# Performance work log

Measured on AMD Instinct MI355X. Metric: run time of the kernel, lower is better.

Reference implementation:

```python
import jax, jax.numpy as jnp
import numpy as np

# Module constants (from init_kwargs / defaults)
OUT_SIZE = (4, 32, 32)      # (Z, X, Y) grid
REAL_SIZE = (3.0, 25.0, 25.0)
SCALE = 1.4
THRESHOLD = 0.5
D_ELEMS = np.array([0.74 * SCALE, 0.528 * SCALE], dtype=np.float32)  # per-element match/NMS radius (O, H)


def _transform(x):
    """(B, X, Y, Z, 4*E) -> coords (B, E, N, 3), conf (B, E, N); N = Z*X*Y."""
    B, X, Y, Z, L = x.shape
    E = L // 4
    v = x.reshape(B, X, Y, Z, E, 4).transpose(0, 4, 3, 1, 2, 5)   # (B,E,Z,X,Y,4)
    v = v[..., jnp.array([2, 0, 1, 3])]                            # reorder last dim
    Zs, Xs, Ys = OUT_SIZE
    ind = jnp.stack(jnp.meshgrid(jnp.arange(Zs), jnp.arange(Xs), jnp.arange(Ys), indexing='ij'),
                    axis=-1).astype(x.dtype)                       # (Z,X,Y,3) == torch nonzero of ones
    expand = jnp.array([r / o for o, r in zip(OUT_SIZE, REAL_SIZE)], dtype=x.dtype)
    coords = (v[..., :3] + ind) * expand
    conf = v[..., 3]
    N = Zs * Xs * Ys
    return coords.reshape(B, E, N, 3), conf.reshape(B, E, N)


def _sort_by_conf(coords, conf):
    order = jnp.argsort(-conf, axis=-1)
    coords = jnp.take_along_axis(coords, order[..., None], axis=2)
    conf = jnp.take_along_axis(conf, order, axis=-1)
    return coords, conf


def _nms(pts, valid, d):
    """Greedy sequential NMS on one (N,3) point set. Point b is suppressed if any
    still-selected earlier point a<b lies within distance d. Invalid points never suppress."""
    N = pts.shape[0]
    d2 = jnp.sum((pts[:, None, :] - pts[None, :, :]) ** 2, axis=-1)   # (N,N)
    ar = jnp.arange(N)
    M = (d2 < d * d) & valid[:, None] & valid[None, :] & (ar[:, None] < ar[None, :])

    def body(b, sel):
        return sel.at[b].set(~jnp.any(sel & M[:, b]))

    sel = jax.lax.fori_loop(0, N, body, jnp.ones((N,), bool))
    return sel & valid


def _match(P, T, keepP, keepT, d):
    """Greedy row-major bipartite matching: each pred (in order) grabs the first
    still-unmatched target within distance d. Returns (TP, FP, FN) masks."""
    N = P.shape[0]
    d2 = jnp.sum((P[:, None, :] - T[None, :, :]) ** 2, axis=-1)      # (N,N)
    D = (d2 < d * d) & keepP[:, None] & keepT[None, :]

    def body(a, carry):
        selP, selT = carry
        avail = D[a] & ~selT
        has = jnp.any(avail)
        j = jnp.argmax(avail)                    # first available target index
        selT = selT.at[j].set(selT[j] | has)
        selP = selP.at[a].set(has)
        return (selP, selT)

    selP, selT = jax.lax.fori_loop(0, N, body,
                                   (jnp.zeros((N,), bool), jnp.zeros((N,), bool)))
    return selP, keepP & ~selP, keepT & ~selT    # TP, FP, FN masks


def setup_inputs() -> dict:
    key = jax.random.key(0)
    k1, k2 = jax.random.split(key)
    B = 4
    predictions = jax.random.normal(k1, (B, 32, 32, 4, 8), dtype=jnp.float32)
    targets = jax.random.normal(k2, (B, 32, 32, 4, 8), dtype=jnp.float32)
    return {"predictions": predictions, "targets": targets}


def reference(predictions, targets):
    Pc, Pconf = _sort_by_conf(*_transform(predictions))   # (B,E,N,3), (B,E,N)
    Tc, Tconf = _sort_by_conf(*_transform(targets))
    validP = Pconf > THRESHOLD
    validT = Tconf > THRESHOLD
    d = jnp.asarray(D_ELEMS)                               # (E,)

    nms_be = jax.vmap(jax.vmap(_nms, in_axes=(0, 0, 0)), in_axes=(0, 0, None))
    keepP = nms_be(Pc, validP, d)                          # (B,E,N) bool
    keepT = nms_be(Tc, validT, d)

    match_be = jax.vmap(jax.vmap(_match, in_axes=(0, 0, 0, 0, 0)), in_axes=(0, 0, 0, 0, None))
    tp, fp, fn = match_be(Pc, Tc, keepP, keepT, d)         # (B,E,N) bool each

    # sorted real-space points, NMS-kept masks, and TP/FP/FN masks (fixed-shape
    # equivalents of the torch module's filtered P/T/TP/FP/FN lists)
    return Pc, Tc, keepP, keepT, tp, fp, fn
```

## Files before the change

### kernel.cpp

```cpp
#include <hip/hip_runtime.h>
#include <hip/hip_bf16.h>

#pragma clang fp contract(off)

#define NPTS 4096
#define BE   8
#define COORD_SZ (BE * NPTS * 3)
#define MASK_SZ  (BE * NPTS)
#define OFF_PC   0
#define OFF_TC   (COORD_SZ)
#define OFF_KP   (2 * COORD_SZ)
#define OFF_KT   (2 * COORD_SZ + MASK_SZ)
#define OFF_TP   (2 * COORD_SZ + 2 * MASK_SZ)
#define OFF_FP   (2 * COORD_SZ + 3 * MASK_SZ)
#define OFF_FN   (2 * COORD_SZ + 4 * MASK_SZ)

#define VCAP 1664
#define NW   26

#define WS_V_OFF     524288ull
#define WS_KEEP_OFF  524352ull
#define WS_PP_OFF    528448ull
#define WS_PT_OFF    6066240ull
#define WS_NEED      8835136ull

#define NBC 16

typedef unsigned long long u64;

__device__ __forceinline__ float get_dd(int e) {
    const float d0 = (float)(0.74 * 1.4);
    const float d1 = (float)(0.528 * 1.4);
    float d = (e == 0) ? d0 : d1;
    return d * d;
}

__global__ __launch_bounds__(1024)
void sort_kernel(const float* __restrict__ pred,
                 const float* __restrict__ targ,
                 float* __restrict__ out,
                 int* __restrict__ Vcnt) {
    __shared__ u64 bufA[NPTS], bufB[NPTS];
    __shared__ unsigned int hist[1024];
    __shared__ unsigned int offarr[1024];
    __shared__ int wsum[16];
    __shared__ int vtot;
    const int s = blockIdx.x;
    const int arr = s & 1, be = s >> 1;
    const int b = be >> 1, e = be & 1;
    const float* __restrict__ src = arr ? targ : pred;
    const int t = threadIdx.x;
    const int lane = t & 63, wv = t >> 6;

    if (t == 0) vtot = 0;
    for (int n = t; n < NPTS; n += 1024) {
        int z = n >> 10, r = n & 1023, x = r >> 5, y = r & 31;
        int base = (((b * 32 + x) * 32 + y) * 4 + z) * 8 + e * 4;
        float conf = src[base + 3];
        unsigned int bits = __float_as_uint(conf);
        unsigned int u = (bits & 0x80000000u) ? ~bits : (bits | 0x80000000u);
        bufA[n] = ((u64)(~u) << 32) | (unsigned int)n;
    }
    __syncthreads();

    const u64 lmask = (1ull << lane) - 1ull;
    for (int k = 0; k < 8; ++k) {
        u64* cur = (k & 1) ? bufB : bufA;
        u64* nxt = (k & 1) ? bufA : bufB;
        const int shift = 32 + (k << 2);
        hist[t] = 0u;
        __syncthreads();

        u64 item[4]; int dg[4]; int rnk[4];
        #pragma unroll
        for (int m = 0; m < 4; ++m) {
            u64 it = cur[m * 1024 + t];
            int d = (int)((it >> shift) & 15);
            u64 eq = ~0ull;
            #pragma unroll
            for (int bb = 0; bb < 4; ++bb) {
                u64 bal = __ballot((d >> bb) & 1);
                eq &= ((d >> bb) & 1) ? bal : ~bal;
            }
            int r = (int)__popcll(eq & lmask);
            if (r == 0) hist[d * 64 + m * 16 + wv] = (unsigned int)__popcll(eq);
            item[m] = it; dg[m] = d; rnk[m] = r;
        }
        __syncthreads();

        {
            int v = (int)hist[t];
            int inc = v;
            #pragma unroll
            for (int dd = 1; dd < 64; dd <<= 1) {
                int x2 = __shfl_up(inc, dd);
                if (lane >= dd) inc += x2;
            }
            if (lane == 63) wsum[wv] = inc;
            __syncthreads();
            if (t < 16) {
                int wtot = wsum[t]; int iv = wtot;
                #pragma unroll
                for (int dd = 1; dd < 16; dd <<= 1) {
                    int x2 = __shfl_up(iv, dd);
                    if (t >= dd) iv += x2;
                }
                wsum[t] = iv - wtot;
            }
            __syncthreads();
            offarr[t] = (unsigned int)(wsum[wv] + (inc - v));
        }
        __syncthreads();

        #pragma unroll
        for (int m = 0; m < 4; ++m) {
            int pos = (int)offarr[dg[m] * 64 + m * 16 + wv] + rnk[m];
            nxt[pos] = item[m];
        }
        __syncthreads();
    }

    int myv = 0;
    for (int p = t; p < NPTS; p += 1024) {
        u64 key = bufA[p];
        int n = (int)(key & 0xFFFFFFFFull);
        myv += ((unsigned int)(key >> 32) < 0x40FFFFFFu) ? 1 : 0;
        int z = n >> 10, rr = n & 1023, x = rr >> 5, y = rr & 31;
        int base = (((b * 32 + x) * 32 + y) * 4 + z) * 8 + e * 4;
        float r0 = src[base + 0], r1 = src[base + 1], r2 = src[base + 2];
        float c0 = (r2 + (float)z) * 0.75f;
        float c1 = (r0 + (float)x) * 0.78125f;
        float c2 = (r1 + (float)y) * 0.78125f;
        float* dst = out + (size_t)arr * COORD_SZ + ((size_t)be * NPTS + p) * 3;
        dst[0] = c0; dst[1] = c1; dst[2] = c2;
    }
    atomicAdd(&vtot, myv);
    __syncthreads();
    if (t == 0) Vcnt[s] = vtot;
}

__global__ __launch_bounds__(256)
void matrix_kernel(const float* __restrict__ out,
                   const int* __restrict__ Vcnt,
                   u64* __restrict__ ws64) {
    __shared__ float4 tcol[VCAP];
    __shared__ float rowc[64][3];
    const int bx = blockIdx.x;
    const int j = bx / 26, c = bx % 26;
    const int t = threadIdx.x;

    int sRow, sCol, e;
    u64* dstBase;
    if (j < 16) {
        sRow = j; sCol = j; e = (j >> 1) & 1;
        dstBase = ws64 + (WS_PP_OFF / 8) + (size_t)j * VCAP * NW;
    } else {
        int be = j - 16;
        sRow = be * 2 + 0; sCol = be * 2 + 1; e = be & 1;
        dstBase = ws64 + (WS_PT_OFF / 8) + (size_t)be * VCAP * NW;
    }
    int Vr = Vcnt[sRow]; if (Vr > VCAP) Vr = VCAP;
    int Vc = Vcnt[sCol]; if (Vc > VCAP) Vc = VCAP;
    const int rb = c * 64;
    if (rb >= Vr) return;
    const float dd = get_dd(e);

    const float* __restrict__ colc = out + (size_t)(sCol & 1) * COORD_SZ + (size_t)(sCol >> 1) * NPTS * 3;
    const float* __restrict__ rowp = out + (size_t)(sRow & 1) * COORD_SZ + (size_t)(sRow >> 1) * NPTS * 3;

    for (int idx = t; idx < Vc * 3; idx += 256) {
        float v = colc[idx];
        int p = idx / 3, k = idx % 3;
        ((float*)&tcol[p])[k] = v;
    }
    for (int idx = t; idx < 192; idx += 256) {
        int i = idx / 3, k = idx % 3;
        if (rb + i < Vr) rowc[i][k] = rowp[(rb + i) * 3 + k];
    }
    __syncthreads();

    const int NWc = (Vc + 63) >> 6;
    const int wlimit = (j < 16) ? (c + 1) : NWc;
    const int i = t & 63;
    const bool rowOK = (rb + i) < Vr;
    if (rowOK) {
        float ax = rowc[i][0], ay = rowc[i][1], az = rowc[i][2];
        for (int w = t >> 6; w < wlimit; w += 4) {
            int jbase = w << 6;
            int jmax = Vc - jbase; if (jmax > 64) jmax = 64;
            u64 m = 0ull;
            for (int jj = 0; jj < jmax; ++jj) {
                float4 tc = tcol[jbase + jj];
                float dx = ax - tc.x, dy = ay - tc.y, dz = az - tc.z;
                float d2 = dx * dx + dy * dy + dz * dz;
                m |= (d2 < dd) ? (1ull << jj) : 0ull;
            }
            dstBase[(size_t)w * VCAP + (rb + i)] = m;
        }
    }
}

__global__ __launch_bounds__(1024)
void nms_rounds_kernel(float* __restrict__ out,
                       const int* __restrict__ Vcnt,
                       u64* __restrict__ ws64) {
    __shared__ unsigned short nbr[VCAP][NBC];
    __shared__ unsigned short nbrcnt[VCAP];
    __shared__ u64 U[NW];
    __shared__ u64 K[NW];
    __shared__ int remaining;
    const int s = blockIdx.x;
    const int arr = s & 1, be = s >> 1;
    const int t = threadIdx.x;
    int V = Vcnt[s]; if (V > VCAP) V = VCAP;
    const u64* __restrict__ Mx = ws64 + (WS_PP_OFF / 8) + (size_t)s * VCAP * NW;

    if (t < NW) {
        int rem = V - (t << 6);
        U[t] = (rem >= 64) ? ~0ull : ((rem > 0) ? ((1ull << rem) - 1ull) : 0ull);
        K[t] = 0ull;
    }
    if (t == 0) remaining = V;
    __syncthreads();

    bool dec0 = false, dec1 = false;
    #pragma unroll
    for (int half = 0; half < 2; ++half) {
        const int i = t + half * 1024;
        if (i < V) {
            const int wi = i >> 6;
            int cnt = 0;
            for (int w = 0; w <= wi; ++w) {
                u64 m = Mx[(size_t)w * VCAP + i];
                if (w == wi) m &= (1ull << (i & 63)) - 1ull;
                while (m) {
                    int bb = (int)__builtin_ctzll(m); m &= m - 1ull;
                    if (cnt < NBC) nbr[i][cnt] = (unsigned short)((w << 6) + bb);
                    cnt++;
                }
            }
            nbrcnt[i] = (unsigned short)cnt;
            if (cnt == 0) { if (half == 0) dec0 = true; else dec1 = true; }
        }
    }
    __syncthreads();
    {
        int ndec = 0;
        if (dec0) {
            const int i = t;
            atomicAnd(&U[i >> 6], ~(1ull << (i & 63)));
            atomicOr(&K[i >> 6], 1ull << (i & 63));
            ndec++;
        }
        if (dec1) {
            const int i = t + 1024;
            atomicAnd(&U[i >> 6], ~(1ull << (i & 63)));
            atomicOr(&K[i >> 6], 1ull << (i & 63));
            ndec++;
        }
        if (ndec) atomicSub(&remaining, ndec);
    }
    __syncthreads();

    while (remaining > 0) {
        bool d0 = false, k0 = false, d1 = false, k1 = false;
        #pragma unroll
        for (int half = 0; half < 2; ++half) {
            const int i = t + half * 1024;
            if (i < V && ((U[i >> 6] >> (i & 63)) & 1ull)) {
                bool cu = false, ck = false;
                int cnt = nbrcnt[i];
                if (cnt <= NBC) {
                    for (int k = 0; k < cnt; ++k) {
                        int j = nbr[i][k];
                        u64 bit = 1ull << (j & 63);
                        cu = cu || ((U[j >> 6] & bit) != 0ull);
                        ck = ck || ((K[j >> 6] & bit) != 0ull);
                    }
                } else {
                    const int wi = i >> 6;
                    u64 cuw = 0ull, ckw = 0ull;
                    for (int w = 0; w <= wi; ++w) {
                        u64 m = Mx[(size_t)w * VCAP + i];
                        if (w == wi) m &= (1ull << (i & 63)) - 1ull;
                        cuw |= m & U[w];
                        ckw |= m & K[w];
                    }
                    cu = cuw != 0ull; ck = ckw != 0ull;
                }
                if (!cu) {
                    if (half == 0) { d0 = true; k0 = !ck; }
                    else           { d1 = true; k1 = !ck; }
                }
            }
        }
        __syncthreads();

        int ndec = 0;
        if (d0) {
            const int i = t;
            atomicAnd(&U[i >> 6], ~(1ull << (i & 63)));
            if (k0) atomicOr(&K[i >> 6], 1ull << (i & 63));
            ndec++;
        }
        if (d1) {
            const int i = t + 1024;
            atomicAnd(&U[i >> 6], ~(1ull << (i & 63)));
            if (k1) atomicOr(&K[i >> 6], 1ull << (i & 63));
            ndec++;
        }
        if (ndec) atomicSub(&remaining, ndec);
        __syncthreads();
    }

    u64* kb = ws64 + (WS_KEEP_OFF / 8) + s * 32;
    if (t < 32) kb[t] = (t < NW) ? K[t] : 0ull;
    const size_t kbase = (arr == 0 ? OFF_KP : OFF_KT) + (size_t)be * NPTS;
    for (int p = t; p < NPTS; p += 1024) {
        bool k = (p < V) && ((K[p >> 6] >> (p & 63)) & 1ull);
        out[kbase + p] = k ? 1.0f : 0.0f;
    }
}

__global__ __launch_bounds__(1024)
void match_resolve_kernel(float* __restrict__ out,
                          const int* __restrict__ Vcnt,
                          u64* __restrict__ ws64) {
    __shared__ unsigned short cand[VCAP][16];
    __shared__ unsigned short candcnt[VCAP];
    __shared__ unsigned short rowlist[VCAP];
    __shared__ unsigned int colmin[VCAP];
    __shared__ u64 kPw[NW], kTw[NW], availT[NW];
    __shared__ int wp[NW];
    __shared__ int Mcnt, remaining;
    __shared__ unsigned int selP32[128];
    const int be = blockIdx.x;
    const int t = threadIdx.x;
    int Vp = Vcnt[be * 2 + 0]; if (Vp > VCAP) Vp = VCAP;
    int Vt = Vcnt[be * 2 + 1]; if (Vt > VCAP) Vt = VCAP;
    const int NWt = (Vt + 63) >> 6;
    const u64* __restrict__ PT = ws64 + (WS_PT_OFF / 8) + (size_t)be * VCAP * NW;

    if (t < NW) {
        kPw[t] = ws64[(WS_KEEP_OFF / 8) + (be * 2 + 0) * 32 + t];
        kTw[t] = ws64[(WS_KEEP_OFF / 8) + (be * 2 + 1) * 32 + t];
    }
    if (t < 128) selP32[t] = 0u;
    for (int idx = t; idx < VCAP; idx += 1024) colmin[idx] = 0xFFFFFFFFu;
    __syncthreads();

    if (t < 64) {
        int cP = (t < NW) ? __popcll(kPw[t]) : 0;
        int o = cP;
        for (int d = 1; d < 64; d <<= 1) {
            int v = __shfl_up(o, d);
            if (t >= d) o += v;
        }
        if (t < NW) wp[t] = o - cP;
        if (t == NW - 1) Mcnt = o;
    }
    __syncthreads();
    const int M = Mcnt;

    for (int a = t; a < Vp; a += 1024) {
        int w = a >> 6, bb = a & 63;
        u64 word = kPw[w];
        if ((word >> bb) & 1ull) {
            int pos = wp[w] + __popcll(word & ((1ull << bb) - 1ull));
            rowlist[pos] = (unsigned short)a;
        }
    }
    if (t < NW) availT[t] = kTw[t];
    if (t == 0) remaining = M;
    __syncthreads();

    #pragma unroll
    for (int half = 0; half < 2; ++half) {
        int g = t + half * 1024;
        if (g < M) {
            const int a = rowlist[g];
            int cnt = 0;
            for (int w = 0; w < NWt; ++w) {
                u64 m = PT[(size_t)w * VCAP + a] & kTw[w];
                while (m) {
                    int bb = (int)__builtin_ctzll(m); m &= m - 1ull;
                    if (cnt < 16) cand[g][cnt] = (unsigned short)((w << 6) + bb);
                    cnt++;
                }
            }
            candcnt[g] = (unsigned short)(cnt > 16 ? 16 : cnt);
        }
    }
    __syncthreads();

    bool und0 = (t < M);
    bool und1 = (t + 1024 < M);
    int round = 0;

    while (remaining > 0) {
        const unsigned int stampBase = (unsigned int)(4095 - round) << 11;
        int jt0 = -1, jt1 = -1;
        bool dead0 = false, dead1 = false;
        if (und0) {
            const int g = t;
            int cn = candcnt[g];
            for (int k = 0; k < cn; ++k) {
                int j = cand[g][k];
                if ((availT[j >> 6] >> (j & 63)) & 1ull) {
                    if (jt0 < 0) jt0 = j;
                    atomicMin(&colmin[j], stampBase | (unsigned int)g);
                }
            }
            if (jt0 < 0) dead0 = true;
        }
        if (und1) {
            const int g = t + 1024;
            int cn = candcnt[g];
            for (int k = 0; k < cn; ++k) {
                int j = cand[g][k];
                if ((availT[j >> 6] >> (j & 63)) & 1ull) {
                    if (jt1 < 0) jt1 = j;
                    atomicMin(&colmin[j], stampBase | (unsigned int)g);
                }
            }
            if (jt1 < 0) dead1 = true;
        }
        __syncthreads();

        int ndec = 0;
        if (und0) {
            const int g = t;
            if (dead0) { und0 = false; ndec++; }
            else if (colmin[jt0] == (stampBase | (unsigned int)g)) {
                atomicAnd(&availT[jt0 >> 6], ~(1ull << (jt0 & 63)));
                int a = rowlist[g];
                atomicOr(&selP32[a >> 5], 1u << (a & 31));
                und0 = false; ndec++;
            }
        }
        if (und1) {
            const int g = t + 1024;
            if (dead1) { und1 = false; ndec++; }
            else if (colmin[jt1] == (stampBase | (unsigned int)g)) {
                atomicAnd(&availT[jt1 >> 6], ~(1ull << (jt1 & 63)));
                int a = rowlist[g];
                atomicOr(&selP32[a >> 5], 1u << (a & 31));
                und1 = false; ndec++;
            }
        }
        if (ndec) atomicSub(&remaining, ndec);
        ++round;
        __syncthreads();
    }

    for (int n = t; n < NPTS; n += 1024) {
        int w = n >> 6;
        bool kpb = (w < NW) && ((kPw[w] >> (n & 63)) & 1ull);
        bool tpb = (selP32[n >> 5] >> (n & 31)) & 1u;
        bool fnb = (w < NW) && ((availT[w] >> (n & 63)) & 1ull);
        size_t o = (size_t)be * NPTS + n;
        out[OFF_TP + o] = tpb ? 1.0f : 0.0f;
        out[OFF_FP + o] = (kpb && !tpb) ? 1.0f : 0.0f;
        out[OFF_FN + o] = fnb ? 1.0f : 0.0f;
    }
}

#define FVCAP 2048
#define FNWMAX (FVCAP / 64)

__global__ __launch_bounds__(1024)
void sortnms_fallback(const float* __restrict__ pred,
                      const float* __restrict__ targ,
                      float* __restrict__ out,
                      u64* __restrict__ keepbits) {
    __shared__ u64 skey[NPTS];
    __shared__ float px[FVCAP], py[FVCAP], pz[FVCAP];
    __shared__ u64 kept[FNWMAX];
    __shared__ u64 mchunk[64];
    __shared__ int supp[64];
    __shared__ int vcnt;
    const int blk = blockIdx.x;
    const int arr = blk & 1;
    const int be  = blk >> 1;
    const int b = be >> 1, e = be & 1;
    const float* __restrict__ src = arr ? targ : pred;
    const int t = threadIdx.x;
    const float dd = get_dd(e);
    if (t == 0) vcnt = 0;

    for (int n = t; n < NPTS; n += 1024) {
        int z = n >> 10, r = n & 1023, x = r >> 5, y = r & 31;
        int base = (((b * 32 + x) * 32 + y) * 4 + z) * 8 + e * 4;
        float conf = src[base + 3];
        unsigned int bits = __float_as_uint(conf);
        unsigned int u = (bits & 0x80000000u) ? ~bits : (bits | 0x80000000u);
        skey[n] = ((u64)(~u) << 32) | (unsigned int)n;
    }
    __syncthreads();
    for (int k = 2; k <= NPTS; k <<= 1) {
        for (int j = k >> 1; j > 0; j >>= 1) {
            for (int i = t; i < NPTS; i += 1024) {
                int ixj = i ^ j;
                if (ixj > i) {
                    u64 a = skey[i], c = skey[ixj];
                    bool up = ((i & k) == 0);
                    if ((a > c) == up) { skey[i] = c; skey[ixj] = a; }
                }
            }
            __syncthreads();
        }
    }
    int myv = 0;
    for (int p = t; p < NPTS; p += 1024) {
        u64 key = skey[p];
        int n = (int)(key & 0xFFFFFFFFu);
        unsigned int u = ~(unsigned int)(key >> 32);
        myv += (u > 0xBF000000u) ? 1 : 0;
        int z = n >> 10, r = n & 1023, x = r >> 5, y = r & 31;
        int base = (((b * 32 + x) * 32 + y) * 4 + z) * 8 + e * 4;
        float r0 = src[base + 0], r1 = src[base + 1], r2 = src[base + 2];
        float c0 = (r2 + (float)z) * 0.75f;
        float c1 = (r0 + (float)x) * 0.78125f;
        float c2 = (r1 + (float)y) * 0.78125f;
        float* dst = out + (size_t)arr * COORD_SZ + ((size_t)be * NPTS + p) * 3;
        dst[0] = c0; dst[1] = c1; dst[2] = c2;
        if (p < FVCAP) { px[p] = c0; py[p] = c1; pz[p] = c2; }
    }
    atomicAdd(&vcnt, myv);
    if (t < FNWMAX) kept[t] = 0ull;
    __syncthreads();

    int V = vcnt; if (V > FVCAP) V = FVCAP;
    const int nchunks = (V + 63) >> 6;
    for (int c = 0; c < nchunks; ++c) {
        if (t < 64) supp[t] = 0;
        __syncthreads();
        {
            int i = t & 63, s = t >> 6;
            int p = (c << 6) + i;
            if (p < V) {
                float x = px[p], y = py[p], z = pz[p];
                int lim = c << 6;
                bool f = false;
                for (int j = s; j < lim; j += 16) {
                    if ((kept[j >> 6] >> (j & 63)) & 1ull) {
                        float dx = x - px[j], dy = y - py[j], dz = z - pz[j];
                        float d2 = dx * dx + dy * dy + dz * dz;
                        if (d2 < dd) { f = true; break; }
                    }
                }
                if (f) atomicOr(&supp[i], 1);
            }
        }
        __syncthreads();
        if (t < 64) {
            int p = (c << 6) + t;
            u64 m = 0ull;
            if (p < V) {
                float x = px[p], y = py[p], z = pz[p];
                for (int j = 0; j < t; ++j) {
                    int q = (c << 6) + j;
                    float dx = x - px[q], dy = y - py[q], dz = z - pz[q];
                    float d2 = dx * dx + dy * dy + dz * dz;
                    if (d2 < dd) m |= (1ull << j);
                }
            }
            mchunk[t] = m;
        }
        __syncthreads();
        if (t == 0) {
            u64 kw = 0ull;
            int lim = V - (c << 6); if (lim > 64) lim = 64;
            for (int i = 0; i < lim; ++i) {
                bool ki = (supp[i] == 0) && ((mchunk[i] & kw) == 0ull);
                if (ki) kw |= (1ull << i);
            }
            kept[c] = kw;
        }
        __syncthreads();
    }
    const size_t kbase = (arr == 0 ? OFF_KP : OFF_KT) + (size_t)be * NPTS;
    for (int p = t; p < NPTS; p += 1024) {
        bool kb = (p < V) && ((kept[(p >> 6) & (FNWMAX - 1)] >> (p & 63)) & 1ull);
        out[kbase + p] = kb ? 1.0f : 0.0f;
    }
    if (t < 64) keepbits[blk * 64 + t] = (t < FNWMAX) ? kept[t] : 0ull;
}

__global__ __launch_bounds__(1024)
void match_fallback(float* __restrict__ out,
                    const u64* __restrict__ keepbits) {
    __shared__ float tx[FVCAP], ty[FVCAP], tz[FVCAP];
    __shared__ unsigned short tj[FVCAP];
    __shared__ unsigned short aidx[FVCAP];
    __shared__ unsigned short matchPos[FVCAP];
    __shared__ u64 Mask[64][FNWMAX + 1];
    __shared__ u64 kPm[64], kTm[64];
    __shared__ unsigned int selP32[128], selT32[128];
    __shared__ int wpT[64], wpP[64];
    __shared__ int Mcnt2, Kcnt2;
    __shared__ float pcx[64], pcy[64], pcz[64];
    const int be = blockIdx.x;
    const int e = be & 1;
    const int t = threadIdx.x;
    const float dd = get_dd(e);
    const float* __restrict__ Pc = out + OFF_PC + (size_t)be * NPTS * 3;
    const float* __restrict__ Tc = out + OFF_TC + (size_t)be * NPTS * 3;

    if (t < 64) {
        kPm[t] = keepbits[(be * 2 + 0) * 64 + t];
        kTm[t] = keepbits[(be * 2 + 1) * 64 + t];
    }
    if (t < 128) { selP32[t] = 0u; selT32[t] = 0u; }
    __syncthreads();
    if (t < 64) {
        int cT = __popcll(kTm[t]), cP = __popcll(kPm[t]);
        int oT = cT, oP = cP;
        for (int d = 1; d < 64; d <<= 1) {
            int vT = __shfl_up(oT, d);
            int vP = __shfl_up(oP, d);
            if (t >= d) { oT += vT; oP += vP; }
        }
        wpT[t] = oT - cT;
        wpP[t] = oP - cP;
        if (t == 63) {
            Kcnt2 = (oT > FVCAP) ? FVCAP : oT;
            Mcnt2 = (oP > FVCAP) ? FVCAP : oP;
        }
    }
    __syncthreads();
    const int K = Kcnt2, M = Mcnt2;
    for (int n = t; n < NPTS; n += 1024) {
        int w = n >> 6, bb = n & 63;
        u64 bit = 1ull << bb, lowm = bit - 1ull;
        u64 wT = kTm[w], wP = kPm[w];
        if (wT & bit) {
            int pos = wpT[w] + __popcll(wT & lowm);
            if (pos < FVCAP) {
                tx[pos] = Tc[n * 3 + 0];
                ty[pos] = Tc[n * 3 + 1];
                tz[pos] = Tc[n * 3 + 2];
                tj[pos] = (unsigned short)n;
            }
        }
        if (wP & bit) {
            int pos = wpP[w] + __popcll(wP & lowm);
            if (pos < FVCAP) aidx[pos] = (unsigned short)n;
        }
    }
    __syncthreads();

    const int NWc = (K + 63) >> 6;
    const int nchunks = (M + 63) >> 6;
    u64 selTw = 0ull;

    for (int c = 0; c < nchunks; ++c) {
        int cnt = M - (c << 6); if (cnt > 64) cnt = 64;
        if (t < 64 && t < cnt) {
            int a = aidx[(c << 6) + t];
            pcx[t] = Pc[a * 3 + 0];
            pcy[t] = Pc[a * 3 + 1];
            pcz[t] = Pc[a * 3 + 2];
        }
        __syncthreads();
        {
            int i = t & 63, s = t >> 6;
            if (i < cnt) {
                float ax = pcx[i], ay = pcy[i], az = pcz[i];
                for (int w = s; w < NWc; w += 16) {
                    int jmax = K - (w << 6); if (jmax > 64) jmax = 64;
                    int base = w << 6;
                    u64 m = 0ull;
                    for (int jj = 0; jj < jmax; ++jj) {
                        float dx = ax - tx[base + jj];
                        float dy = ay - ty[base + jj];
                        float dz = az - tz[base + jj];
                        float d2 = dx * dx + dy * dy + dz * dz;
                        m |= (d2 < dd) ? (1ull << jj) : 0ull;
                    }
                    Mask[i][w] = m;
                }
            }
        }
        __syncthreads();
        if (t < 64) {
            u64 mnext = (cnt > 0 && t < NWc) ? Mask[0][t] : 0ull;
            for (int i = 0; i < cnt; ++i) {
                u64 mrow = mnext;
                mnext = (i + 1 < cnt && t < NWc) ? Mask[i + 1][t] : 0ull;
                u64 avail = mrow & ~selTw;
                u64 bal = __ballot(avail != 0ull);
                if (bal) {
                    int w0 = (int)__builtin_ctzll(bal);
                    if (t == w0) {
                        int bb = (int)__builtin_ctzll(avail);
                        selTw |= 1ull << bb;
                        matchPos[(c << 6) + i] = (unsigned short)((w0 << 6) + bb);
                    }
                } else if (t == 0) {
                    matchPos[(c << 6) + i] = 0xffffu;
                }
            }
        }
        __syncthreads();
    }
    for (int g = t; g < M; g += 1024) {
        unsigned short pos = matchPos[g];
        if (pos != 0xffffu) {
            int jj = tj[pos];
            int a  = aidx[g];
            atomicOr(&selT32[jj >> 5], 1u << (jj & 31));
            atomicOr(&selP32[a >> 5],  1u << (a & 31));
        }
    }
    __syncthreads();
    for (int n = t; n < NPTS; n += 1024) {
        bool kpb = (kPm[n >> 6] >> (n & 63)) & 1ull;
        bool ktb = (kTm[n >> 6] >> (n & 63)) & 1ull;
        bool tpb = (selP32[n >> 5] >> (n & 31)) & 1u;
        bool stb = (selT32[n >> 5] >> (n & 31)) & 1u;
        size_t o = (size_t)be * NPTS + n;
        out[OFF_TP + o] = tpb ? 1.0f : 0.0f;
        out[OFF_FP + o] = (kpb && !tpb) ? 1.0f : 0.0f;
        out[OFF_FN + o] = (ktb && !stb) ? 1.0f : 0.0f;
    }
}

extern "C" void kernel_launch(void* const* d_in, const int* in_sizes, int n_in,
                              void* d_out, int out_size, void* d_ws, size_t ws_size,
                              hipStream_t stream) {
    const float* pred = (const float*)d_in[0];
    const float* targ = (const float*)d_in[1];
    float* out = (float*)d_out;

    if (ws_size >= WS_NEED) {
        int* Vcnt = (int*)((char*)d_ws + WS_V_OFF);
        u64* ws64 = (u64*)d_ws;

        sort_kernel<<<16, 1024, 0, stream>>>(pred, targ, out, Vcnt);
        matrix_kernel<<<624, 256, 0, stream>>>(out, Vcnt, ws64);
        nms_rounds_kernel<<<16, 1024, 0, stream>>>(out, Vcnt, ws64);
        match_resolve_kernel<<<8, 1024, 0, stream>>>(out, Vcnt, ws64);
    } else {
        u64* keepbits = (u64*)d_ws;
        sortnms_fallback<<<16, 1024, 0, stream>>>(pred, targ, out, keepbits);
        match_fallback<<<8, 1024, 0, stream>>>(out, keepbits);
    }
}
```

Baseline: 161.2 us.

## Use per-point byte state with in-round updates in NMS rounds kernel

Replaces the shared U/K bitmasks in the NMS rounds loop with a volatile per-point byte state (undecided, kept, suppressed). Points write their decision as soon as they make it, so later points in the same round can see it. A point is now suppressed as soon as any earlier neighbour is kept, without waiting for every neighbour to be decided. This drops one barrier per round, removes the 64-bit atomics, and should need fewer rounds. The keep bitmask is rebuilt with wave ballots at the end. The risk is that correctness now depends on state changes only ever moving forward and on volatile visibility across waves.

```diff
diff --git a/kernel.cpp b/kernel.cpp
--- a/kernel.cpp
+++ b/kernel.cpp
@@ -206,24 +206,21 @@
                        u64* __restrict__ ws64) {
     __shared__ unsigned short nbr[VCAP][NBC];
     __shared__ unsigned short nbrcnt[VCAP];
-    __shared__ u64 U[NW];
-    __shared__ u64 K[NW];
+    __shared__ unsigned char stbuf[VCAP];
     __shared__ int remaining;
+    volatile unsigned char* st = stbuf;
     const int s = blockIdx.x;
     const int arr = s & 1, be = s >> 1;
     const int t = threadIdx.x;
     int V = Vcnt[s]; if (V > VCAP) V = VCAP;
     const u64* __restrict__ Mx = ws64 + (WS_PP_OFF / 8) + (size_t)s * VCAP * NW;
 
-    if (t < NW) {
-        int rem = V - (t << 6);
-        U[t] = (rem >= 64) ? ~0ull : ((rem > 0) ? ((1ull << rem) - 1ull) : 0ull);
-        K[t] = 0ull;
-    }
+    for (int i = t; i < VCAP; i += 1024) stbuf[i] = 0;
     if (t == 0) remaining = V;
     __syncthreads();
 
-    bool dec0 = false, dec1 = false;
+    bool und0 = (t < V), und1 = (t + 1024 < V);
+    int ndec1 = 0;
     #pragma unroll
     for (int half = 0; half < 2; ++half) {
         const int i = t + half * 1024;
@@ -240,84 +237,67 @@
                 }
             }
             nbrcnt[i] = (unsigned short)cnt;
-            if (cnt == 0) { if (half == 0) dec0 = true; else dec1 = true; }
-        }
-    }
-    __syncthreads();
-    {
+            if (cnt == 0) {
+                st[i] = 1;
+                if (half == 0) und0 = false; else und1 = false;
+                ndec1++;
+            }
+        }
+    }
+    if (ndec1) atomicSub(&remaining, ndec1);
+    __syncthreads();
+
+    while (remaining > 0) {
         int ndec = 0;
-        if (dec0) {
-            const int i = t;
-            atomicAnd(&U[i >> 6], ~(1ull << (i & 63)));
-            atomicOr(&K[i >> 6], 1ull << (i & 63));
-            ndec++;
-        }
-        if (dec1) {
-            const int i = t + 1024;
-            atomicAnd(&U[i >> 6], ~(1ull << (i & 63)));
-            atomicOr(&K[i >> 6], 1ull << (i & 63));
-            ndec++;
-        }
-        if (ndec) atomicSub(&remaining, ndec);
-    }
-    __syncthreads();
-
-    while (remaining > 0) {
-        bool d0 = false, k0 = false, d1 = false, k1 = false;
         #pragma unroll
         for (int half = 0; half < 2; ++half) {
-            const int i = t + half * 1024;
-            if (i < V && ((U[i >> 6] >> (i & 63)) & 1ull)) {
+            bool& und = (half == 0) ? und0 : und1;
+            if (und) {
+                const int i = t + half * 1024;
                 bool cu = false, ck = false;
                 int cnt = nbrcnt[i];
                 if (cnt <= NBC) {
                     for (int k = 0; k < cnt; ++k) {
-                        int j = nbr[i][k];
-                        u64 bit = 1ull << (j & 63);
-                        cu = cu || ((U[j >> 6] & bit) != 0ull);
-                        ck = ck || ((K[j >> 6] & bit) != 0ull);
+                        int sj = st[nbr[i][k]];
+                        ck = ck || (sj == 1);
+                        cu = cu || (sj == 0);
                     }
                 } else {
                     const int wi = i >> 6;
-                    u64 cuw = 0ull, ckw = 0ull;
                     for (int w = 0; w <= wi; ++w) {
                         u64 m = Mx[(size_t)w * VCAP + i];
                         if (w == wi) m &= (1ull << (i & 63)) - 1ull;
-                        cuw |= m & U[w];
-                        ckw |= m & K[w];
+                        while (m) {
+                            int bb = (int)__builtin_ctzll(m); m &= m - 1ull;
+                            int sj = st[(w << 6) + bb];
+                            ck = ck || (sj == 1);
+                            cu = cu || (sj == 0);
+                        }
                     }
-                    cu = cuw != 0ull; ck = ckw != 0ull;
-                }
-                if (!cu) {
-                    if (half == 0) { d0 = true; k0 = !ck; }
-                    else           { d1 = true; k1 = !ck; }
-                }
-            }
-        }
-        __syncthreads();
-
-        int ndec = 0;
-        if (d0) {
-            const int i = t;
-            atomicAnd(&U[i >> 6], ~(1ull << (i & 63)));
-            if (k0) atomicOr(&K[i >> 6], 1ull << (i & 63));
-            ndec++;
-        }
-        if (d1) {
-            const int i = t + 1024;
-            atomicAnd(&U[i >> 6], ~(1ull << (i & 63)));
-            if (k1) atomicOr(&K[i >> 6], 1ull << (i & 63));
-            ndec++;
+                }
+                if (ck) {
+                    st[i] = 2;
+                    und = false; ndec++;
+                } else if (!cu) {
+                    st[i] = 1;
+                    und = false; ndec++;
+                }
+            }
         }
         if (ndec) atomicSub(&remaining, ndec);
         __syncthreads();
     }
 
+    u64 wlo = __ballot((t < V) && (st[t] == 1));
+    u64 whi = __ballot((t + 1024 < V) && (st[t + 1024] == 1));
     u64* kb = ws64 + (WS_KEEP_OFF / 8) + s * 32;
-    if (t < 32) kb[t] = (t < NW) ? K[t] : 0ull;
+    if ((t & 63) == 0) {
+        kb[t >> 6] = wlo;
+        kb[16 + (t >> 6)] = whi;
+    }
     const size_t kbase = (arr == 0 ? OFF_KP : OFF_KT) + (size_t)be * NPTS;
     for (int p = t; p < NPTS; p += 1024) {
-        bool k = (p < V) && ((K[p >> 6] >> (p & 63)) & 1ull);
+        bool k = (p < V) && (st[p] == 1);
         out[kbase + p] = k ? 1.0f : 0.0f;
     }
 }
```

Measured after the change: 149.3 us. -7.4%, faster.
